# Kernel tuning notes

Measured on AMD Instinct MI355X. Metric: run time of the kernel, lower is better.

Reference implementation:

```python
import jax, jax.numpy as jnp
import numpy as np


def _rope(x):
    # x: [B*, L, Dh] with Dh even
    L, Dh = x.shape[-2], x.shape[-1]
    inv = 1.0 / (10000.0 ** (jnp.arange(0, Dh, 2, dtype=jnp.float32) / Dh))
    freq = jnp.arange(L, dtype=jnp.float32)[:, None] * inv[None, :]  # [L, Dh/2]
    emb = jnp.concatenate([freq, freq], axis=-1)                     # [L, Dh]
    cos_, sin_ = jnp.cos(emb), jnp.sin(emb)
    half = Dh // 2
    x_rot = jnp.concatenate([-x[..., half:], x[..., :half]], axis=-1)
    return x * cos_ + x_rot * sin_


def setup_inputs() -> dict:
    key = jax.random.key(0)
    k1, k2, k3 = jax.random.split(key, 3)
    B, L, D = 2, 2048, 1024
    x = jax.random.normal(k1, (B, L, D), dtype=jnp.float32)
    key_mask = jnp.ones((B, L), dtype=jnp.int32)
    w_qkv = jax.random.normal(k2, (D, 3 * D), dtype=jnp.float32) * (D ** -0.5)
    w_proj = jax.random.normal(k3, (D, D), dtype=jnp.float32) * (D ** -0.5)
    return {"x": x, "key_mask": key_mask, "w_qkv": w_qkv, "w_proj": w_proj}


def reference(x, key_mask, w_qkv, w_proj):
    B, L, D = x.shape
    H = 16
    Dh = D // H
    scale = Dh ** -0.5
    qkv = (x @ w_qkv).reshape(B, L, 3, H, Dh).transpose(2, 0, 3, 1, 4)  # [3,B,H,L,Dh]
    q, k, v = qkv[0], qkv[1], qkv[2]
    q = _rope(q)
    k = _rope(k)
    sc = jnp.einsum('bhqd,bhkd->bhqk', q, k) * scale  # [B,H,L,L]
    sc = jnp.where(key_mask[:, None, None, :] == 0, -jnp.inf, sc)
    w = jax.nn.softmax(sc, axis=-1)
    out = jnp.einsum('bhqk,bhkd->bhqd', w, v)  # [B,H,L,Dh]
    out = out.transpose(0, 2, 1, 3).reshape(B, L, D)
    return out @ w_proj
```

## Files before the change

kernel.cpp:

```cpp
#include <hip/hip_runtime.h>
#include <hip/hip_bf16.h>
#include <math.h>


typedef __attribute__((ext_vector_type(8))) short bf16x8;
typedef __attribute__((ext_vector_type(4))) float f32x4;
typedef __attribute__((ext_vector_type(16))) float f32x16;

__device__ __forceinline__ unsigned short f2bf(float f) {
    union { float f; unsigned int u; } v; v.f = f;
    unsigned int u = v.u;
    return (unsigned short)((u + 0x7FFFu + ((u >> 16) & 1u)) >> 16);
}

__device__ __forceinline__ unsigned short bfc(float f) {
    union { __hip_bfloat16 h; unsigned short u; } c;
    c.h = __float2bfloat16(f);
    return c.u;
}

__device__ __forceinline__ unsigned cvtpk(float a, float b) {
    unsigned r;
    asm("v_cvt_pk_bf16_f32 %0, %1, %2" : "=v"(r) : "v"(a), "v"(b));
    return r;
}

__device__ __forceinline__ void gload_lds16(const unsigned short* g, unsigned short* l) {
    __builtin_amdgcn_global_load_lds(
        (const __attribute__((address_space(1))) void*)g,
        (__attribute__((address_space(3))) void*)l, 16, 0, 0);
}

__global__ __launch_bounds__(256) void prep_all(
    const float* __restrict__ x, const float* __restrict__ w_qkv, const float* __restrict__ w_proj,
    const int* __restrict__ mask,
    unsigned short* __restrict__ xsw, unsigned short* __restrict__ wqT,
    unsigned short* __restrict__ wpT, float2* __restrict__ tab,
    unsigned long long* __restrict__ mb)
{
    __shared__ unsigned short t[32][34];
    int bid = blockIdx.x, tid = threadIdx.x;
    if (bid < 2048) {
        int i = bid * 256 + tid;
        int row = i >> 7, blk = i & 127;
        int swblk = (blk & ~7) | ((blk ^ row) & 7);
        const float* src = x + ((size_t)row << 10) + (blk << 3);
        float4 f0 = *(const float4*)(src);
        float4 f1 = *(const float4*)(src + 4);
        ushort4 h0, h1;
        h0.x = f2bf(f0.x); h0.y = f2bf(f0.y); h0.z = f2bf(f0.z); h0.w = f2bf(f0.w);
        h1.x = f2bf(f1.x); h1.y = f2bf(f1.y); h1.z = f2bf(f1.z); h1.w = f2bf(f1.w);
        ushort4* dst = (ushort4*)(xsw + ((size_t)row << 10) + (swblk << 3));
        dst[0] = h0; dst[1] = h1;
    } else if (bid < 6144) {
        const float* w; unsigned short* wT; int Ncols, u;
        if (bid < 5120) { w = w_qkv; wT = wqT; Ncols = 3072; u = bid - 2048; }
        else            { w = w_proj; wT = wpT; Ncols = 1024; u = bid - 5120; }
        int NBx = Ncols >> 5;
        int n0 = (u % NBx) * 32, k0 = (u / NBx) * 32;
        int r = tid >> 3, c4 = (tid & 7) * 4;
        float4 f = *(const float4*)(w + (size_t)(k0 + r) * Ncols + n0 + c4);
        t[c4 + 0][r] = f2bf(f.x);
        t[c4 + 1][r] = f2bf(f.y);
        t[c4 + 2][r] = f2bf(f.z);
        t[c4 + 3][r] = f2bf(f.w);
        __syncthreads();
        ushort4 o;
        o.x = t[r][c4]; o.y = t[r][c4 + 1]; o.z = t[r][c4 + 2]; o.w = t[r][c4 + 3];
        int n = n0 + r, k = k0 + c4;
        int ksw = (k & ~63) | ((((k >> 3) ^ n) & 7) << 3) | (k & 7);
        *(ushort4*)(wT + (size_t)n * 1024 + ksw) = o;
    } else if (bid < 6400) {
        int i = (bid - 6144) * 256 + tid;
        int pos = i >> 5, d = i & 31;
        float inv = expf(-0.28782313662f * (float)d);
        float ang = (float)pos * inv;
        float s, c;
        sincosf(ang, &s, &c);
        tab[i] = make_float2(c, s);
    } else if (tid < 64) {
        int b = tid >> 5, w = tid & 31;
        unsigned long long bits = 0;
        #pragma unroll 8
        for (int j = 0; j < 64; ++j)
            if (mask[b * 2048 + w * 64 + j]) bits |= (1ULL << j);
        mb[tid] = bits;
    }
}

template<int MODE>
__global__ __launch_bounds__(256) void gemm_kernel(
    const unsigned short* __restrict__ Asw, const unsigned short* __restrict__ BT,
    const float2* __restrict__ ropetab,
    unsigned short* __restrict__ qb, unsigned short* __restrict__ kb,
    unsigned short* __restrict__ vb, float* __restrict__ Cout, int NB)
{
    const int K = 1024;
    __shared__ __align__(16) unsigned short As[128 * 64];
    __shared__ __align__(16) unsigned short Bs[64 * 64];
    int tid = threadIdx.x;
    int wid = tid >> 6, lane = tid & 63, lr = lane & 15, lg = lane >> 4;
    int wm = wid * 32;

    int per = NB * 4;
    int flat = blockIdx.x;
    int w = (flat & 7) * per + (flat >> 3);
    int row0 = (w / NB) * 128, col0 = (w % NB) * 64;

    int swk = (lr & 7) << 3;

    f32x4 acc[2][4];
    #pragma unroll
    for (int m = 0; m < 2; ++m)
        #pragma unroll
        for (int n = 0; n < 4; ++n)
            #pragma unroll
            for (int i = 0; i < 4; ++i) acc[m][n][i] = 0.0f;

    for (int k0 = 0; k0 < K; k0 += 64) {
        #pragma unroll
        for (int i = 0; i < 2; ++i) {
            int cbase = (i * 4 + wid) * 64;
            int c = cbase + lane;
            int r = c >> 3, cc = (c & 7) * 8;
            gload_lds16(BT + (size_t)(col0 + r) * K + k0 + cc, Bs + cbase * 8);
        }
        #pragma unroll
        for (int i = 0; i < 4; ++i) {
            int cbase = (i * 4 + wid) * 64;
            int c = cbase + lane;
            int r = c >> 3, cc = (c & 7) * 8;
            gload_lds16(Asw + (size_t)(row0 + r) * K + k0 + cc, As + cbase * 8);
        }
        __syncthreads();
        #pragma unroll
        for (int kk = 0; kk < 2; ++kk) {
            bf16x8 af[2], bfr[4];
            #pragma unroll
            for (int m = 0; m < 2; ++m)
                af[m] = *(const bf16x8*)(&As[(wm + m * 16 + lr) * 64 + ((kk * 32 + lg * 8) ^ swk)]);
            #pragma unroll
            for (int n = 0; n < 4; ++n)
                bfr[n] = *(const bf16x8*)(&Bs[(n * 16 + lr) * 64 + ((kk * 32 + lg * 8) ^ swk)]);
            #pragma unroll
            for (int m = 0; m < 2; ++m)
                #pragma unroll
                for (int n = 0; n < 4; ++n)
                    acc[m][n] = __builtin_amdgcn_mfma_f32_16x16x32_bf16(af[m], bfr[n], acc[m][n], 0, 0, 0);
        }
        __syncthreads();
    }

    if (MODE == 1) {
        int N = NB * 64;
        #pragma unroll
        for (int m = 0; m < 2; ++m)
            #pragma unroll
            for (int reg = 0; reg < 4; ++reg) {
                int grow = row0 + wm + m * 16 + lg * 4 + reg;
                #pragma unroll
                for (int n = 0; n < 4; ++n)
                    Cout[(size_t)grow * N + col0 + n * 16 + lr] = acc[m][n][reg];
            }
    } else {
        #pragma unroll
        for (int m = 0; m < 2; ++m)
            #pragma unroll
            for (int reg = 0; reg < 4; ++reg) {
                int grow = row0 + wm + m * 16 + lg * 4 + reg;
                int pos = grow & 2047;
                int bb = grow >> 11;
                #pragma unroll
                for (int n = 0; n < 4; ++n) {
                    int col = col0 + n * 16 + lr;
                    int part = col >> 10;
                    int h = (col >> 6) & 15;
                    int d = col & 63;
                    float v0 = acc[m][n][reg];
                    if (part == 2) {
                        int posl = (pos & 63) ^ ((d & 7) << 3);
                        vb[((size_t)bb * 16 + h) * 131072 + (size_t)d * 2048 + (pos & ~63) + posl] = f2bf(v0);
                    } else if (n < 2) {
                        float v1 = acc[m][n + 2][reg];
                        float2 cs = ropetab[pos * 32 + d];
                        size_t base = (((size_t)bb * 16 + h) * 2048 + pos) * 64;
                        float e0 = v0 * cs.x - v1 * cs.y;
                        float e1 = v1 * cs.x + v0 * cs.y;
                        if (part == 0) {
                            qb[base + d]      = f2bf(e0 * 0.18033688f);
                            qb[base + d + 32] = f2bf(e1 * 0.18033688f);
                        } else {
                            int sw = (pos & 7) << 3;
                            kb[base + (d ^ sw)]        = f2bf(e0);
                            kb[base + ((d + 32) ^ sw)] = f2bf(e1);
                        }
                    }
                }
            }
    }
}

__global__ __launch_bounds__(256, 2) void attn_kernel(
    const unsigned short* __restrict__ qbuf, const unsigned short* __restrict__ kbuf,
    const unsigned short* __restrict__ vtbuf, const unsigned long long* __restrict__ mbits,
    unsigned short* __restrict__ obuf)
{
    __shared__ __align__(16) unsigned short Ks[3][4096];
    __shared__ __align__(16) unsigned short Vs[3][4096];

    int flat = blockIdx.x;
    int w = ((flat & 7) << 6) + (flat >> 3);
    int bh = w >> 4, qt = w & 15;
    int b = bh >> 4, h = bh & 15;
    int tid = threadIdx.x, wid = tid >> 6, lane = tid & 63;
    int l31 = lane & 31, hi = lane >> 5, hi8 = hi << 3;
    int qrow0 = qt * 128 + wid * 32;
    const size_t bhbase = (size_t)bh * (2048 * 64);
    const unsigned short* kB = kbuf + bhbase;
    const unsigned short* vt = vtbuf + bhbase;
    const unsigned long long* mw = mbits + (b << 5);
    int swl = (l31 & 7) << 3;

    bf16x8 qf[4];
    #pragma unroll
    for (int s = 0; s < 4; ++s)
        qf[s] = *(const bf16x8*)(qbuf + bhbase + (size_t)(qrow0 + l31) * 64 + s * 16 + hi8);

    f32x16 oacc[2];
    #pragma unroll
    for (int db = 0; db < 2; ++db)
        #pragma unroll
        for (int i = 0; i < 16; ++i) oacc[db][i] = 0.0f;
    float mrow = -INFINITY, lrow = 0.f;
    bf16x8 pfp[4];

    auto stage = [&](int t, unsigned short* Kb, unsigned short* Vb) {
        #pragma unroll
        for (int i = 0; i < 2; ++i) {
            int idx = i * 256 + tid;
            gload_lds16(kB + (size_t)t * 4096 + idx * 8, Kb + i * 2048 + wid * 512);
            gload_lds16(vt + (size_t)(idx >> 3) * 2048 + t * 64 + (idx & 7) * 8, Vb + i * 2048 + wid * 512);
        }
    };

    unsigned short *Kcur = Ks[0], *Knxt = Ks[1], *Kprv = Ks[2];
    unsigned short *Vcur = Vs[0], *Vnxt = Vs[1], *Vprv = Vs[2];

    stage(0, Kcur, Vcur);
    #pragma unroll 1
    for (int t = 0; t < 32; ++t) {
        __syncthreads();
        if (t < 31) stage(t + 1, Knxt, Vnxt);
        unsigned long long bb = mw[t];

        __builtin_amdgcn_s_setprio(1);
        f32x16 sacc[2];
        #pragma unroll
        for (int ka = 0; ka < 2; ++ka)
            #pragma unroll
            for (int i = 0; i < 16; ++i) sacc[ka][i] = 0.0f;
        #pragma unroll
        for (int s = 0; s < 4; ++s)
            #pragma unroll
            for (int ka = 0; ka < 2; ++ka) {
                bf16x8 kfx = *(const bf16x8*)(Kcur + (ka * 32 + l31) * 64 + ((s * 16 + hi8) ^ swl));
                sacc[ka] = __builtin_amdgcn_mfma_f32_32x32x16_bf16(kfx, qf[s], sacc[ka], 0, 0, 0);
            }
        if (t) {
            #pragma unroll
            for (int s = 0; s < 4; ++s)
                #pragma unroll
                for (int db = 0; db < 2; ++db) {
                    bf16x8 vfx = *(const bf16x8*)(Vprv + (db * 32 + l31) * 64 + ((s * 16 + hi8) ^ swl));
                    oacc[db] = __builtin_amdgcn_mfma_f32_32x32x16_bf16(pfp[s], vfx, oacc[db], 0, 0, 0);
                }
        }
        __builtin_amdgcn_s_setprio(0);

        if (bb != ~0ULL) {
            int hi4 = hi << 2;
            #pragma unroll
            for (int kb = 0; kb < 2; ++kb)
                #pragma unroll
                for (int reg = 0; reg < 16; ++reg) {
                    int kv = kb * 32 + (reg & 3) + ((reg >> 2) << 3) + hi4;
                    if (!((bb >> kv) & 1)) sacc[kb][reg] = -1e30f;
                }
        }

        float tmax = sacc[0][0];
        #pragma unroll
        for (int kb = 0; kb < 2; ++kb)
            #pragma unroll
            for (int reg = 0; reg < 16; ++reg)
                if (kb | reg) tmax = fmaxf(tmax, sacc[kb][reg]);
        tmax = fmaxf(tmax, __shfl_xor(tmax, 32));

        if (__any(tmax > mrow + 8.f)) {
            float mnew = fmaxf(mrow, tmax);
            float sc = (mrow == -INFINITY) ? 0.f : __builtin_amdgcn_exp2f(mrow - mnew);
            lrow *= sc;
            mrow = mnew;
            #pragma unroll
            for (int reg = 0; reg < 16; ++reg) {
                int qof = (reg & 3) + ((reg >> 2) << 3) + (hi << 2);
                float scq = __shfl(sc, qof);
                oacc[0][reg] *= scq;
                oacc[1][reg] *= scq;
            }
        }

        float ps = 0.f;
        #pragma unroll
        for (int kb = 0; kb < 2; ++kb)
            #pragma unroll
            for (int reg = 0; reg < 16; ++reg) {
                float pv = __builtin_amdgcn_exp2f(sacc[kb][reg] - mrow);
                sacc[kb][reg] = pv;
                ps += pv;
            }
        lrow += ps;

        #pragma unroll
        for (int s = 0; s < 4; ++s) {
            int kb = s >> 1, ra = (s & 1) * 8;
            unsigned wA0 = cvtpk(sacc[kb][ra + 0], sacc[kb][ra + 1]);
            unsigned wA1 = cvtpk(sacc[kb][ra + 2], sacc[kb][ra + 3]);
            unsigned wB0 = cvtpk(sacc[kb][ra + 4], sacc[kb][ra + 5]);
            unsigned wB1 = cvtpk(sacc[kb][ra + 6], sacc[kb][ra + 7]);
            asm("v_permlane32_swap_b32 %0, %1" : "+v"(wA0), "+v"(wB0));
            asm("v_permlane32_swap_b32 %0, %1" : "+v"(wA1), "+v"(wB1));
            union { unsigned u[4]; bf16x8 v; } pk;
            pk.u[0] = wA0; pk.u[1] = wA1; pk.u[2] = wB0; pk.u[3] = wB1;
            pfp[s] = pk.v;
        }

        unsigned short* tK = Kprv; Kprv = Kcur; Kcur = Knxt; Knxt = tK;
        unsigned short* tV = Vprv; Vprv = Vcur; Vcur = Vnxt; Vnxt = tV;
    }

    #pragma unroll
    for (int s = 0; s < 4; ++s)
        #pragma unroll
        for (int db = 0; db < 2; ++db) {
            bf16x8 vfx = *(const bf16x8*)(Vprv + (db * 32 + l31) * 64 + ((s * 16 + hi8) ^ swl));
            oacc[db] = __builtin_amdgcn_mfma_f32_32x32x16_bf16(pfp[s], vfx, oacc[db], 0, 0, 0);
        }

    lrow += __shfl_xor(lrow, 32);

    #pragma unroll
    for (int reg = 0; reg < 16; ++reg) {
        int qof = (reg & 3) + ((reg >> 2) << 3) + (hi << 2);
        float lq = __shfl(lrow, qof);
        float linv = 1.0f / lq;
        int qrow = qrow0 + qof;
        int qsw = qrow & 7;
        #pragma unroll
        for (int db = 0; db < 2; ++db) {
            int dcol = db * 32 + l31;
            int jj = dcol >> 3;
            int colsw = h * 64 + (((jj ^ qsw) & 7) << 3) + (dcol & 7);
            obuf[((size_t)b * 2048 + qrow) * 1024 + colsw] = bfc(oacc[db][reg] * linv);
        }
    }
}

extern "C" void kernel_launch(void* const* d_in, const int* in_sizes, int n_in,
                              void* d_out, int out_size, void* d_ws, size_t ws_size,
                              hipStream_t stream) {
    const float* x      = (const float*)d_in[0];
    const int* key_mask = (const int*)d_in[1];
    const float* w_qkv  = (const float*)d_in[2];
    const float* w_proj = (const float*)d_in[3];
    float* out = (float*)d_out;

    char* ws = (char*)d_ws;
    unsigned short* qb  = (unsigned short*)(ws);
    unsigned short* kb  = (unsigned short*)(ws + 8388608);
    unsigned short* vtb = (unsigned short*)(ws + 16777216);
    unsigned short* xob = (unsigned short*)(ws + 25165824);
    unsigned short* wqT = (unsigned short*)(ws + 33554432);
    unsigned short* wpT = (unsigned short*)(ws + 39845888);
    float2*         tab = (float2*)(ws + 41943040);
    unsigned long long* mb = (unsigned long long*)(ws + 42467328);

    dim3 blk(256);
    prep_all<<<dim3(6401), blk, 0, stream>>>(x, w_qkv, w_proj, key_mask, xob, wqT, wpT, tab, mb);
    gemm_kernel<0><<<dim3(1536), blk, 0, stream>>>(xob, wqT, tab, qb, kb, vtb, nullptr, 48);
    attn_kernel<<<dim3(512), blk, 0, stream>>>(qb, kb, vtb, mb, xob);
    gemm_kernel<1><<<dim3(512), blk, 0, stream>>>(xob, wpT, nullptr, nullptr, nullptr, nullptr, out, 16);
}
```

Baseline: 122.2 us.

## Split attention KV range across two wave groups and merge softmax partials via LDS

Each attention block now runs 512 threads. The two halves of four waves each process half of the key/value sequence (16 tiles each instead of 32) with separate LDS staging buffers. At the end the second half writes its O accumulator, row max and row sum to shared memory, and the first half rescales and combines them before writing the output. This halves the serial loop length per wave and raises active waves per CU. In exchange it adds an LDS exchange, an extra barrier, more shared memory per block, and launch bounds of (512,4), which may constrain registers.

Measured after the change: 135.0 us. +10.5%, slower.

```diff
diff --git a/kernel.cpp b/kernel.cpp
--- a/kernel.cpp
+++ b/kernel.cpp
@@ -200,26 +200,32 @@
     }
 }
 
-__global__ __launch_bounds__(256, 2) void attn_kernel(
+__global__ __launch_bounds__(512, 4) void attn_kernel(
     const unsigned short* __restrict__ qbuf, const unsigned short* __restrict__ kbuf,
     const unsigned short* __restrict__ vtbuf, const unsigned long long* __restrict__ mbits,
     unsigned short* __restrict__ obuf)
 {
-    __shared__ __align__(16) unsigned short Ks[3][4096];
-    __shared__ __align__(16) unsigned short Vs[3][4096];
+    __shared__ __align__(16) unsigned short S[2][20480];
 
     int flat = blockIdx.x;
     int w = ((flat & 7) << 6) + (flat >> 3);
     int bh = w >> 4, qt = w & 15;
     int b = bh >> 4, h = bh & 15;
-    int tid = threadIdx.x, wid = tid >> 6, lane = tid & 63;
+    int tid = threadIdx.x;
+    int wid = tid >> 6;
+    int half = wid >> 2, wq = wid & 3;
+    int lane = tid & 63;
     int l31 = lane & 31, hi = lane >> 5, hi8 = hi << 3;
-    int qrow0 = qt * 128 + wid * 32;
+    int ht = tid & 255;
+    int qrow0 = qt * 128 + wq * 32;
     const size_t bhbase = (size_t)bh * (2048 * 64);
-    const unsigned short* kB = kbuf + bhbase;
+    const unsigned short* kB = kbuf + bhbase + ((size_t)half << 16);
     const unsigned short* vt = vtbuf + bhbase;
-    const unsigned long long* mw = mbits + (b << 5);
+    const unsigned long long* mw = mbits + (b << 5) + (half << 4);
     int swl = (l31 & 7) << 3;
+
+    unsigned short* Kb = S[half];
+    unsigned short* Vb = S[half] + 8192;
 
     bf16x8 qf[4];
     #pragma unroll
@@ -234,24 +240,25 @@
     float mrow = -INFINITY, lrow = 0.f;
     bf16x8 pfp[4];
 
-    auto stage = [&](int t, unsigned short* Kb, unsigned short* Vb) {
+    auto stage = [&](int t, int kbi, int vbi) {
         #pragma unroll
         for (int i = 0; i < 2; ++i) {
-            int idx = i * 256 + tid;
-            gload_lds16(kB + (size_t)t * 4096 + idx * 8, Kb + i * 2048 + wid * 512);
-            gload_lds16(vt + (size_t)(idx >> 3) * 2048 + t * 64 + (idx & 7) * 8, Vb + i * 2048 + wid * 512);
+            int idx = i * 256 + ht;
+            gload_lds16(kB + (size_t)t * 4096 + idx * 8, Kb + kbi * 4096 + i * 2048 + wq * 512);
+            gload_lds16(vt + (size_t)(idx >> 3) * 2048 + (half * 16 + t) * 64 + (idx & 7) * 8,
+                        Vb + vbi * 4096 + i * 2048 + wq * 512);
         }
     };
 
-    unsigned short *Kcur = Ks[0], *Knxt = Ks[1], *Kprv = Ks[2];
-    unsigned short *Vcur = Vs[0], *Vnxt = Vs[1], *Vprv = Vs[2];
-
-    stage(0, Kcur, Vcur);
+    int vc = 0, vn = 1, vp = 2;
+    stage(0, 0, vc);
     #pragma unroll 1
-    for (int t = 0; t < 32; ++t) {
+    for (int t = 0; t < 16; ++t) {
         __syncthreads();
-        if (t < 31) stage(t + 1, Knxt, Vnxt);
+        if (t < 15) stage(t + 1, (t + 1) & 1, vn);
         unsigned long long bb = mw[t];
+        const unsigned short* Kcur = Kb + (t & 1) * 4096;
+        const unsigned short* Vprv = Vb + vp * 4096;
 
         __builtin_amdgcn_s_setprio(1);
         f32x16 sacc[2];
@@ -280,20 +287,20 @@
         if (bb != ~0ULL) {
             int hi4 = hi << 2;
             #pragma unroll
-            for (int kb = 0; kb < 2; ++kb)
+            for (int kb2 = 0; kb2 < 2; ++kb2)
                 #pragma unroll
                 for (int reg = 0; reg < 16; ++reg) {
-                    int kv = kb * 32 + (reg & 3) + ((reg >> 2) << 3) + hi4;
-                    if (!((bb >> kv) & 1)) sacc[kb][reg] = -1e30f;
+                    int kv = kb2 * 32 + (reg & 3) + ((reg >> 2) << 3) + hi4;
+                    if (!((bb >> kv) & 1)) sacc[kb2][reg] = -1e30f;
                 }
         }
 
         float tmax = sacc[0][0];
         #pragma unroll
-        for (int kb = 0; kb < 2; ++kb)
+        for (int kb2 = 0; kb2 < 2; ++kb2)
             #pragma unroll
             for (int reg = 0; reg < 16; ++reg)
-                if (kb | reg) tmax = fmaxf(tmax, sacc[kb][reg]);
+                if (kb2 | reg) tmax = fmaxf(tmax, sacc[kb2][reg]);
         tmax = fmaxf(tmax, __shfl_xor(tmax, 32));
 
         if (__any(tmax > mrow + 8.f)) {
@@ -312,22 +319,22 @@
 
         float ps = 0.f;
         #pragma unroll
-        for (int kb = 0; kb < 2; ++kb)
+        for (int kb2 = 0; kb2 < 2; ++kb2)
             #pragma unroll
             for (int reg = 0; reg < 16; ++reg) {
-                float pv = __builtin_amdgcn_exp2f(sacc[kb][reg] - mrow);
-                sacc[kb][reg] = pv;
+                float pv = __builtin_amdgcn_exp2f(sacc[kb2][reg] - mrow);
+                sacc[kb2][reg] = pv;
                 ps += pv;
             }
         lrow += ps;
 
         #pragma unroll
         for (int s = 0; s < 4; ++s) {
-            int kb = s >> 1, ra = (s & 1) * 8;
-            unsigned wA0 = cvtpk(sacc[kb][ra + 0], sacc[kb][ra + 1]);
-            unsigned wA1 = cvtpk(sacc[kb][ra + 2], sacc[kb][ra + 3]);
-            unsigned wB0 = cvtpk(sacc[kb][ra + 4], sacc[kb][ra + 5]);
-            unsigned wB1 = cvtpk(sacc[kb][ra + 6], sacc[kb][ra + 7]);
+            int kb2 = s >> 1, ra = (s & 1) * 8;
+            unsigned wA0 = cvtpk(sacc[kb2][ra + 0], sacc[kb2][ra + 1]);
+            unsigned wA1 = cvtpk(sacc[kb2][ra + 2], sacc[kb2][ra + 3]);
+            unsigned wB0 = cvtpk(sacc[kb2][ra + 4], sacc[kb2][ra + 5]);
+            unsigned wB1 = cvtpk(sacc[kb2][ra + 6], sacc[kb2][ra + 7]);
             asm("v_permlane32_swap_b32 %0, %1" : "+v"(wA0), "+v"(wB0));
             asm("v_permlane32_swap_b32 %0, %1" : "+v"(wA1), "+v"(wB1));
             union { unsigned u[4]; bf16x8 v; } pk;
@@ -335,33 +342,60 @@
             pfp[s] = pk.v;
         }
 
-        unsigned short* tK = Kprv; Kprv = Kcur; Kcur = Knxt; Knxt = tK;
-        unsigned short* tV = Vprv; Vprv = Vcur; Vcur = Vnxt; Vnxt = tV;
-    }
-
-    #pragma unroll
-    for (int s = 0; s < 4; ++s)
-        #pragma unroll
-        for (int db = 0; db < 2; ++db) {
-            bf16x8 vfx = *(const bf16x8*)(Vprv + (db * 32 + l31) * 64 + ((s * 16 + hi8) ^ swl));
-            oacc[db] = __builtin_amdgcn_mfma_f32_32x32x16_bf16(pfp[s], vfx, oacc[db], 0, 0, 0);
-        }
-
+        int tmp = vp; vp = vc; vc = vn; vn = tmp;
+    }
+
+    {
+        const unsigned short* Vprv = Vb + vp * 4096;
+        #pragma unroll
+        for (int s = 0; s < 4; ++s)
+            #pragma unroll
+            for (int db = 0; db < 2; ++db) {
+                bf16x8 vfx = *(const bf16x8*)(Vprv + (db * 32 + l31) * 64 + ((s * 16 + hi8) ^ swl));
+                oacc[db] = __builtin_amdgcn_mfma_f32_32x32x16_bf16(pfp[s], vfx, oacc[db], 0, 0, 0);
+            }
+    }
     lrow += __shfl_xor(lrow, 32);
 
-    #pragma unroll
-    for (int reg = 0; reg < 16; ++reg) {
-        int qof = (reg & 3) + ((reg >> 2) << 3) + (hi << 2);
-        float lq = __shfl(lrow, qof);
-        float linv = 1.0f / lq;
-        int qrow = qrow0 + qof;
-        int qsw = qrow & 7;
-        #pragma unroll
-        for (int db = 0; db < 2; ++db) {
-            int dcol = db * 32 + l31;
-            int jj = dcol >> 3;
-            int colsw = h * 64 + (((jj ^ qsw) & 7) << 3) + (dcol & 7);
-            obuf[((size_t)b * 2048 + qrow) * 1024 + colsw] = bfc(oacc[db][reg] * linv);
+    __syncthreads();
+    float* xO = (float*)&S[0][0];
+    float* xm = xO + 8192;
+    float* xl = xm + 256;
+    if (half == 1) {
+        float* dst = xO + (wq * 64 + lane) * 32;
+        #pragma unroll
+        for (int db = 0; db < 2; ++db)
+            #pragma unroll
+            for (int reg = 0; reg < 16; ++reg)
+                dst[db * 16 + reg] = oacc[db][reg];
+        xm[wq * 64 + lane] = mrow;
+        xl[wq * 64 + lane] = lrow;
+    }
+    __syncthreads();
+    if (half == 0) {
+        float m1 = xm[wq * 64 + lane];
+        float l1 = xl[wq * 64 + lane];
+        float mst = fmaxf(mrow, m1);
+        float a0 = (mrow == -INFINITY) ? 0.f : __builtin_amdgcn_exp2f(mrow - mst);
+        float a1 = (m1 == -INFINITY) ? 0.f : __builtin_amdgcn_exp2f(m1 - mst);
+        float lst = lrow * a0 + l1 * a1;
+        const float* src = xO + (wq * 64 + lane) * 32;
+        #pragma unroll
+        for (int reg = 0; reg < 16; ++reg) {
+            int qof = (reg & 3) + ((reg >> 2) << 3) + (hi << 2);
+            float s0 = __shfl(a0, qof);
+            float s1 = __shfl(a1, qof);
+            float li = 1.0f / __shfl(lst, qof);
+            int qrow = qrow0 + qof;
+            int qsw = qrow & 7;
+            #pragma unroll
+            for (int db = 0; db < 2; ++db) {
+                float val = (oacc[db][reg] * s0 + src[db * 16 + reg] * s1) * li;
+                int dcol = db * 32 + l31;
+                int jj = dcol >> 3;
+                int colsw = h * 64 + (((jj ^ qsw) & 7) << 3) + (dcol & 7);
+                obuf[((size_t)b * 2048 + qrow) * 1024 + colsw] = bfc(val);
+            }
         }
     }
 }
@@ -388,6 +422,6 @@
     dim3 blk(256);
     prep_all<<<dim3(6401), blk, 0, stream>>>(x, w_qkv, w_proj, key_mask, xob, wqT, wpT, tab, mb);
     gemm_kernel<0><<<dim3(1536), blk, 0, stream>>>(xob, wqT, tab, qb, kb, vtb, nullptr, 48);
-    attn_kernel<<<dim3(512), blk, 0, stream>>>(qb, kb, vtb, mb, xob);
+    attn_kernel<<<dim3(512), dim3(512), 0, stream>>>(qb, kb, vtb, mb, xob);
     gemm_kernel<1><<<dim3(512), blk, 0, stream>>>(xob, wpT, nullptr, nullptr, nullptr, nullptr, out, 16);
 }
```
